# Performance work log

Hardware: AMD Instinct MI355X
Metric: run time of the kernel (lower is better)

## Reference

```python
import jax, jax.numpy as jnp
import numpy as np

N_NODES = 100000
N_EDGES = 1600000
D_IN = 128
D_HID = 128
D_OUT = 10
N_GRAPHS = 512


def _sage_conv(x, src, dst, W_l, b_l, W_r, num_nodes):
    # PyG SAGEConv (mean aggr): out = lin_l(mean_{j in N(i)} x_j) + lin_r(x_i)
    msg = x[src]                                            # [E, D] gather
    s = jax.ops.segment_sum(msg, dst, num_segments=num_nodes)
    cnt = jax.ops.segment_sum(jnp.ones((src.shape[0], 1), x.dtype), dst,
                              num_segments=num_nodes)
    mean = s / jnp.maximum(cnt, 1.0)                        # 0 where no neighbors
    return mean @ W_l.T + b_l + x @ W_r.T


def setup_inputs() -> dict:
    key = jax.random.key(0)
    ks = jax.random.split(key, 10)
    glorot = lambda k, o, i: jax.random.normal(k, (o, i), jnp.float32) * (1.0 / np.sqrt(i))
    return {
        "x": jax.random.normal(ks[0], (N_NODES, D_IN), jnp.float32),
        "edge_index": jax.random.randint(ks[1], (2, N_EDGES), 0, N_NODES, jnp.int64),
        "batch": jnp.sort(jax.random.randint(ks[2], (N_NODES,), 0, N_GRAPHS, jnp.int64)),
        "W1_l": glorot(ks[3], D_HID, D_IN),
        "b1": jnp.zeros((D_HID,), jnp.float32),
        "W1_r": glorot(ks[4], D_HID, D_IN),
        "W2_l": glorot(ks[5], D_HID, D_HID),
        "b2": jnp.zeros((D_HID,), jnp.float32),
        "W2_r": glorot(ks[6], D_HID, D_HID),
        "Wf": glorot(ks[7], D_OUT, D_HID),
        "bf": jnp.zeros((D_OUT,), jnp.float32),
    }


def reference(x, edge_index, batch, W1_l, b1, W1_r, W2_l, b2, W2_r, Wf, bf):
    src, dst = edge_index[0], edge_index[1]
    n = x.shape[0]
    h = jax.nn.relu(_sage_conv(x, src, dst, W1_l, b1, W1_r, n))
    h = jax.nn.relu(_sage_conv(h, src, dst, W2_l, b2, W2_r, n))
    # global_mean_pool over graph ids
    gsum = jax.ops.segment_sum(h, batch, num_segments=N_GRAPHS)
    gcnt = jax.ops.segment_sum(jnp.ones((n, 1), h.dtype), batch, num_segments=N_GRAPHS)
    g = gsum / jnp.maximum(gcnt, 1.0)
    logits = g @ Wf.T + bf
    return jax.nn.log_softmax(logits, axis=-1)
```

## Files before the change

### kernel.cpp

```cpp
#include <hip/hip_runtime.h>
#include <hip/hip_bf16.h>

#define N_NODES 100000
#define N_EDGES 1600000
#define N_GRAPHS 512
#define NB 256
#define NPB 391
#define CHUNK 6250
#define STAGE 7680

typedef __attribute__((ext_vector_type(8))) short short8;
typedef __attribute__((ext_vector_type(4))) float f32x4;
typedef __attribute__((ext_vector_type(2))) float f32x2;

__device__ __forceinline__ float b2f(ushort u) {
    union { unsigned int i; float f; } c; c.i = ((unsigned int)u) << 16; return c.f;
}
__device__ __forceinline__ float blo(unsigned int u) {
    union { unsigned int i; float f; } c; c.i = u << 16; return c.f;
}
__device__ __forceinline__ float bhi(unsigned int u) {
    union { unsigned int i; float f; } c; c.i = u & 0xffff0000u; return c.f;
}
__device__ __forceinline__ ushort f2b(float f) {
    union { float f; unsigned int i; } c; c.f = f;
    unsigned int r = (c.i + 0x7fffu + ((c.i >> 16) & 1u)) >> 16;
    return (ushort)r;
}
__device__ __forceinline__ int idx_at(const void* p, long i, int f) {
    return f ? (int)((const long long*)p)[i] : ((const int*)p)[i];
}
__device__ __forceinline__ short8 dec8(const uchar* p) {
    uint2 q = *(const uint2*)p;
    f32x2 d0 = __builtin_amdgcn_cvt_pk_f32_fp8((int)q.x, false);
    f32x2 d1 = __builtin_amdgcn_cvt_pk_f32_fp8((int)q.x, true);
    f32x2 d2 = __builtin_amdgcn_cvt_pk_f32_fp8((int)q.y, false);
    f32x2 d3 = __builtin_amdgcn_cvt_pk_f32_fp8((int)q.y, true);
    short8 s;
    s[0] = (short)f2b(d0.x); s[1] = (short)f2b(d0.y);
    s[2] = (short)f2b(d1.x); s[3] = (short)f2b(d1.y);
    s[4] = (short)f2b(d2.x); s[5] = (short)f2b(d2.y);
    s[6] = (short)f2b(d3.x); s[7] = (short)f2b(d3.y);
    return s;
}

__global__ __launch_bounds__(256) void k_detect(const unsigned int* __restrict__ xw,
                                                const unsigned int* __restrict__ ew,
                                                const int* __restrict__ bw,
                                                int* __restrict__ flags) {
    __shared__ int cf, ce, cb;
    int t = threadIdx.x;
    if (t == 0) { cf = 0; ce = 0; cb = 0; }
    __syncthreads();
    unsigned int w = xw[t];
    unsigned int e = (w >> 7) & 0xffu;
    if (e >= 110u && e <= 130u) atomicAdd(&cf, 1);
    if (t < 128) {
        if (ew[2 * t + 1] != 0u) atomicAdd(&ce, 1);
        if (bw[99001 + 2 * t] != 0) atomicAdd(&cb, 1);
    }
    __syncthreads();
    if (t == 0) {
        flags[0] = (cf >= 128) ? 1 : 0;
        flags[1] = (ce == 0) ? 1 : 0;
        flags[2] = (cb == 0) ? 1 : 0;
    }
}

__global__ __launch_bounds__(256) void k_prep(const void* __restrict__ ei,
                                              const void* __restrict__ x,
                                              ushort* __restrict__ xbf,
                                              unsigned int* __restrict__ xf8,
                                              const void* W1l, const void* W1r,
                                              const void* W2l, const void* W2r,
                                              const void* b1,  const void* b2,
                                              ushort* __restrict__ wbf,
                                              int* __restrict__ blkcnt,
                                              const int* __restrict__ flags) {
    int b = blockIdx.x, t = threadIdx.x;
    if (b < NB) {
        __shared__ int h[NB];
        int f = flags[1];
        for (int j = t; j < NB; j += 256) h[j] = 0;
        __syncthreads();
        int lo = b * CHUNK, hi = lo + CHUNK;
        for (int e = lo + t; e < hi; e += 256) {
            int d = idx_at(ei, (long)N_EDGES + e, f);
            atomicAdd(&h[d / NPB], 1);
        }
        __syncthreads();
        if (t < NB) blkcnt[b * NB + t] = h[t];
    } else if (b < NB + 2048) {
        bool f32src = (flags[0] == 0);
        int vb = b - NB;
        const long nG = (long)N_NODES * 128 / 4;
        for (long g = (long)vb * 256 + t; g < nG; g += 2048L * 256) {
            float v0, v1, v2, v3;
            if (f32src) {
                float4 vv = ((const float4*)x)[g];
                v0 = vv.x; v1 = vv.y; v2 = vv.z; v3 = vv.w;
                unsigned int lo = (unsigned int)f2b(v0) | ((unsigned int)f2b(v1) << 16);
                unsigned int hi = (unsigned int)f2b(v2) | ((unsigned int)f2b(v3) << 16);
                ((uint2*)xbf)[g] = make_uint2(lo, hi);
            } else {
                uint2 q = ((const uint2*)x)[g];
                v0 = blo(q.x); v1 = bhi(q.x); v2 = blo(q.y); v3 = bhi(q.y);
            }
            int r = __builtin_amdgcn_cvt_pk_fp8_f32(v0, v1, 0, false);
            r = __builtin_amdgcn_cvt_pk_fp8_f32(v2, v3, r, true);
            xf8[g] = (unsigned int)r;
        }
    } else {
        int idx = (b - NB - 2048) * 256 + t;
        if (idx >= 65792) return;
        const void* src; int off;
        if      (idx < 16384) { src = W1l; off = idx; }
        else if (idx < 32768) { src = W1r; off = idx - 16384; }
        else if (idx < 49152) { src = W2l; off = idx - 32768; }
        else if (idx < 65536) { src = W2r; off = idx - 49152; }
        else if (idx < 65664) { src = b1;  off = idx - 65536; }
        else                  { src = b2;  off = idx - 65664; }
        wbf[idx] = (flags[0] != 0) ? ((const ushort*)src)[off]
                                   : f2b(((const float*)src)[off]);
    }
}

__global__ __launch_bounds__(NB) void k_bscan(const int* __restrict__ blkcnt,
                                              int* __restrict__ bucketBase,
                                              int* __restrict__ blkbase) {
    __shared__ int s[NB];
    int t = threadIdx.x;
    int tot = 0;
    for (int blk = 0; blk < NB; ++blk) tot += blkcnt[blk * NB + t];
    s[t] = tot; __syncthreads();
    for (int off = 1; off < NB; off <<= 1) {
        int a = (t >= off) ? s[t - off] : 0;
        __syncthreads();
        s[t] += a;
        __syncthreads();
    }
    int excl = s[t] - tot;
    bucketBase[t] = excl;
    if (t == NB - 1) bucketBase[NB] = s[NB - 1];
    int run = excl;
    for (int blk = 0; blk < NB; ++blk) {
        blkbase[blk * NB + t] = run;
        run += blkcnt[blk * NB + t];
    }
}

__global__ __launch_bounds__(256) void k_bin(const void* __restrict__ ei,
                                             const int* __restrict__ blkbase,
                                             int* __restrict__ binned,
                                             const int* __restrict__ flags) {
    __shared__ int bb[NB];
    __shared__ int rank[NB];
    int t = threadIdx.x, blk = blockIdx.x;
    int f = flags[1];
    for (int j = t; j < NB; j += 256) { bb[j] = blkbase[blk * NB + j]; rank[j] = 0; }
    __syncthreads();
    int lo = blk * CHUNK, hi = lo + CHUNK;
    for (int e = lo + t; e < hi; e += 256) {
        int s = idx_at(ei, e, f);
        int d = idx_at(ei, (long)N_EDGES + e, f);
        int b = d / NPB;
        int loc = d - b * NPB;
        int r = atomicAdd(&rank[b], 1);
        binned[bb[b] + r] = s | (loc << 20);
    }
}

__global__ __launch_bounds__(256) void k_csr(const int* __restrict__ binned,
                                             const int* __restrict__ bucketBase,
                                             int* __restrict__ rowptr,
                                             int* __restrict__ csr) {
    __shared__ int cnt[400];
    __shared__ int sc[400];
    __shared__ int sh[256];
    __shared__ int stage[STAGE];
    int t = threadIdx.x, b = blockIdx.x;
    int nodeLo = b * NPB;
    int nC = N_NODES - nodeLo; if (nC > NPB) nC = NPB;
    int eBase = bucketBase[b], eEnd = bucketBase[b + 1];

    for (int j = t; j < 400; j += 256) cnt[j] = 0;
    __syncthreads();
    for (int i = eBase + t; i < eEnd; i += 256)
        atomicAdd(&cnt[binned[i] >> 20], 1);
    __syncthreads();
    int base = t * 2;
    int v0 = (base < 400) ? cnt[base] : 0;
    int v1 = (base + 1 < 400) ? cnt[base + 1] : 0;
    int ssum = v0 + v1;
    sh[t] = ssum; __syncthreads();
    for (int off = 1; off < 256; off <<= 1) {
        int a = (t >= off) ? sh[t - off] : 0;
        __syncthreads();
        sh[t] += a;
        __syncthreads();
    }
    int pre = sh[t] - ssum;
    if (base < 400) sc[base] = pre;
    if (base + 1 < 400) sc[base + 1] = pre + v0;
    __syncthreads();
    for (int j = t; j < nC; j += 256) rowptr[nodeLo + j] = eBase + sc[j];
    if (b == NB - 1) {
        if (t == 0) rowptr[N_NODES] = eEnd;
        if (t < 64) csr[N_EDGES + t] = 0;
    }
    for (int j = t; j < 400; j += 256) cnt[j] = 0;
    __syncthreads();
    for (int i = eBase + t; i < eEnd; i += 256) {
        int p = binned[i];
        int loc = p >> 20;
        int pos = sc[loc] + atomicAdd(&cnt[loc], 1);
        int srcn = p & 0xFFFFF;
        if (pos < STAGE) stage[pos] = srcn;
        else csr[eBase + pos] = srcn;
    }
    __syncthreads();
    int eCnt = eEnd - eBase; if (eCnt > STAGE) eCnt = STAGE;
    for (int j = t; j < eCnt; j += 256) csr[eBase + j] = stage[j];
}

__global__ __launch_bounds__(256) void k_agg(const uint2* __restrict__ x16,
                                             const int* __restrict__ rowptr,
                                             const int* __restrict__ csr,
                                             uint2* __restrict__ mout) {
    int wv = blockIdx.x * 4 + (threadIdx.x >> 6);
    int lane = threadIdx.x & 63;
    int li = lane & 15;
    int node = wv * 4 + (lane >> 4);
    int beg = rowptr[node];
    int end = rowptr[node + 1];
    int deg = end - beg;
    int m = deg;
    m = max(m, __shfl_xor(m, 16));
    m = max(m, __shfl_xor(m, 32));
    int degmax = __builtin_amdgcn_readfirstlane(m);
    float a0 = 0.f, a1 = 0.f, a2 = 0.f, a3 = 0.f;
    float a4 = 0.f, a5 = 0.f, a6 = 0.f, a7 = 0.f;
    for (int j = 0; j < degmax; j += 16) {
        int pos = beg + j + li;
        if (pos > end - 1) pos = (deg > 0) ? end - 1 : 0;
        int vidx = csr[pos];
#pragma unroll
        for (int c = 0; c < 16; c += 8) {
            if (j + c >= degmax) break;
            uint2 p[8];
#pragma unroll
            for (int i = 0; i < 8; ++i) {
                int idx = __shfl(vidx, (c + i) | (lane & 48));
                p[i] = x16[(long)idx * 16 + li];
            }
#pragma unroll
            for (int i = 0; i < 8; ++i) {
                bool ok = (j + c + i < deg);
                unsigned int qx = ok ? p[i].x : 0u;
                unsigned int qy = ok ? p[i].y : 0u;
                f32x2 d0 = __builtin_amdgcn_cvt_pk_f32_fp8((int)qx, false);
                f32x2 d1 = __builtin_amdgcn_cvt_pk_f32_fp8((int)qx, true);
                f32x2 d2 = __builtin_amdgcn_cvt_pk_f32_fp8((int)qy, false);
                f32x2 d3 = __builtin_amdgcn_cvt_pk_f32_fp8((int)qy, true);
                a0 += d0.x; a1 += d0.y; a2 += d1.x; a3 += d1.y;
                a4 += d2.x; a5 += d2.y; a6 += d3.x; a7 += d3.y;
            }
        }
    }
    float s = (deg > 0) ? 1.f / (float)deg : 0.f;
    int r0 = __builtin_amdgcn_cvt_pk_fp8_f32(a0 * s, a1 * s, 0, false);
    r0 = __builtin_amdgcn_cvt_pk_fp8_f32(a2 * s, a3 * s, r0, true);
    int r1 = __builtin_amdgcn_cvt_pk_fp8_f32(a4 * s, a5 * s, 0, false);
    r1 = __builtin_amdgcn_cvt_pk_fp8_f32(a6 * s, a7 * s, r1, true);
    mout[(long)node * 16 + li] = make_uint2((unsigned int)r0, (unsigned int)r1);
}

__global__ __launch_bounds__(256) void k_gemm(const uchar* __restrict__ A0f8,
                                              const ushort* __restrict__ A1a,
                                              const ushort* __restrict__ A1b,
                                              const uchar* __restrict__ A1f8,
                                              const ushort* __restrict__ Wl,
                                              const ushort* __restrict__ Wr,
                                              const ushort* __restrict__ bias,
                                              ushort* __restrict__ outb,
                                              uchar* __restrict__ out8,
                                              const int* __restrict__ flags,
                                              int layer1) {
    __shared__ short Ws[4096 * 8];
    int t = threadIdx.x;
    const ushort* A1 = flags[0] ? A1a : A1b;
#pragma unroll
    for (int i = 0; i < 16; ++i) {
        int f = i * 256 + t;
        int lane = f & 63, kk = (f >> 6) & 7, tile = f >> 9;
        int o = tile * 16 + (lane & 15);
        int k0 = kk * 32 + ((lane >> 4) * 8);
        const ushort* wsrc = (k0 < 128) ? (Wl + o * 128 + k0)
                                        : (Wr + o * 128 + (k0 - 128));
        *(short8*)&Ws[f * 8] = *(const short8*)wsrc;
    }
    __syncthreads();

    int wid = t >> 6, lane = t & 63;
    long nbase = (long)blockIdx.x * 64 + (long)wid * 16;
    int arow = (int)nbase + (lane & 15);
    if (arow >= N_NODES) arow = N_NODES - 1;
    int kq = (lane >> 4) * 8;

    short8 afrag[8];
#pragma unroll
    for (int kk = 0; kk < 8; ++kk) {
        int k0 = kk * 32 + kq;
        if (k0 < 128) {
            afrag[kk] = dec8(A0f8 + (long)arow * 128 + k0);
        } else if (layer1) {
            afrag[kk] = *(const short8*)(A1 + (long)arow * 128 + (k0 - 128));
        } else {
            afrag[kk] = dec8(A1f8 + (long)arow * 128 + (k0 - 128));
        }
    }

#pragma unroll
    for (int tile = 0; tile < 8; ++tile) {
        f32x4 acc = {0.f, 0.f, 0.f, 0.f};
#pragma unroll
        for (int kk = 0; kk < 8; ++kk) {
            short8 bfrag = *(short8*)&Ws[((tile * 8 + kk) * 64 + lane) * 8];
            acc = __builtin_amdgcn_mfma_f32_16x16x32_bf16(afrag[kk], bfrag, acc, 0, 0, 0);
        }
        int o = tile * 16 + (lane & 15);
        float bo = b2f(bias[o]);
#pragma unroll
        for (int r = 0; r < 4; ++r) {
            long node = nbase + (lane >> 4) * 4 + r;
            if (node < N_NODES) {
                float v = acc[r] + bo;
                v = v > 0.f ? v : 0.f;
                if (layer1) {
                    int pp = __builtin_amdgcn_cvt_pk_fp8_f32(v, v, 0, false);
                    out8[node * 128 + o] = (uchar)pp;
                } else {
                    outb[node * 128 + o] = f2b(v);
                }
            }
        }
    }
}

__global__ __launch_bounds__(256) void k_pool_cls(const ushort* __restrict__ h2,
                                                  const void* __restrict__ batch,
                                                  const void* __restrict__ Wf,
                                                  const void* __restrict__ bfv,
                                                  void* __restrict__ outp,
                                                  const int* __restrict__ flags) {
    int g = blockIdx.x, t = threadIdx.x;
    int wid = t >> 6, lane = t & 63;
    bool f32 = (flags[0] == 0);
    int b64 = flags[2];
    __shared__ int rng[2];
    __shared__ float redA[4][64];
    __shared__ float redB[4][64];
    __shared__ float gv[128];
    __shared__ float lg[10];
    if (t < 2) {
        int v = g + t, lo = 0, hi = N_NODES;
        while (lo < hi) {
            int mid = (lo + hi) >> 1;
            if (idx_at(batch, mid, b64) < v) lo = mid + 1; else hi = mid;
        }
        rng[t] = lo;
    }
    __syncthreads();
    int lo = rng[0], hi = rng[1];
    const unsigned int* xr = (const unsigned int*)h2;
    float a0 = 0.f, a1 = 0.f;
    int n = lo + wid;
    for (; n + 28 < hi; n += 32) {
        unsigned int p[8];
#pragma unroll
        for (int i = 0; i < 8; ++i) p[i] = xr[(long)(n + i * 4) * 64 + lane];
#pragma unroll
        for (int i = 0; i < 8; ++i) { a0 += blo(p[i]); a1 += bhi(p[i]); }
    }
    for (; n < hi; n += 4) {
        unsigned int q = xr[(long)n * 64 + lane];
        a0 += blo(q); a1 += bhi(q);
    }
    redA[wid][lane] = a0;
    redB[wid][lane] = a1;
    __syncthreads();
    if (wid == 0) {
        float s0 = redA[0][lane] + redA[1][lane] + redA[2][lane] + redA[3][lane];
        float s1 = redB[0][lane] + redB[1][lane] + redB[2][lane] + redB[3][lane];
        float c = (hi > lo) ? (float)(hi - lo) : 1.f;
        gv[lane * 2]     = s0 / c;
        gv[lane * 2 + 1] = s1 / c;
    }
    __syncthreads();
    if (t < 10) {
        float s = f32 ? ((const float*)bfv)[t] : b2f(((const ushort*)bfv)[t]);
        for (int k = 0; k < 128; ++k) {
            float wv = f32 ? ((const float*)Wf)[t * 128 + k] : b2f(((const ushort*)Wf)[t * 128 + k]);
            s += gv[k] * wv;
        }
        lg[t] = s;
    }
    __syncthreads();
    if (t == 0) {
        float mx = lg[0];
        for (int i = 1; i < 10; ++i) mx = fmaxf(mx, lg[i]);
        float se = 0.f;
        for (int i = 0; i < 10; ++i) se += expf(lg[i] - mx);
        float lse = mx + logf(se);
        for (int i = 0; i < 10; ++i) {
            float v = lg[i] - lse;
            if (f32) ((float*)outp)[g * 10 + i] = v;
            else     ((ushort*)outp)[g * 10 + i] = f2b(v);
        }
    }
}

extern "C" void kernel_launch(void* const* d_in, const int* in_sizes, int n_in,
                              void* d_out, int out_size, void* d_ws, size_t ws_size,
                              hipStream_t stream) {
    const void* x     = d_in[0];
    const void* ei    = d_in[1];
    const void* batch = d_in[2];
    const void* W1l = d_in[3];
    const void* b1  = d_in[4];
    const void* W1r = d_in[5];
    const void* W2l = d_in[6];
    const void* b2  = d_in[7];
    const void* W2r = d_in[8];
    const void* Wf  = d_in[9];
    const void* bf_ = d_in[10];

    char* w = (char*)d_ws;
    int* flags      = (int*)(w + 0);
    int* rowptr     = (int*)(w + 640);
    ushort* wbf     = (ushort*)(w + 400768);
    int* csr        = (int*)(w + 532480);
    ushort* xbf     = (ushort*)(w + 6933248);
    ushort* h2      = (ushort*)(w + 6933248);
    uchar* mbuf     = (uchar*)(w + 32533248);
    int* bucketBase = (int*)(w + 32533248);
    int* blkcnt     = (int*)(w + 32534528);
    int* blkbase    = (int*)(w + 32796672);
    uchar* h1f8     = (uchar*)(w + 58133248);
    int* binned     = (int*)(w + 58133248);
    unsigned int* xf8 = (unsigned int*)(w + 70933248);

    dim3 blk256(256), blkNB(NB);

    k_detect<<<1, blk256, 0, stream>>>((const unsigned int*)x, (const unsigned int*)ei,
                                       (const int*)batch, flags);
    k_prep<<<NB + 2048 + 257, blk256, 0, stream>>>(ei, x, xbf, xf8,
                                                   W1l, W1r, W2l, W2r, b1, b2,
                                                   wbf, blkcnt, flags);
    k_bscan<<<1, blkNB, 0, stream>>>(blkcnt, bucketBase, blkbase);
    k_bin<<<NB, blk256, 0, stream>>>(ei, blkbase, binned, flags);
    k_csr<<<NB, blk256, 0, stream>>>(binned, bucketBase, rowptr, csr);

    int agrid = N_NODES / 4 / 4;
    int ggrid = (N_NODES + 63) / 64;

    k_agg<<<agrid, blk256, 0, stream>>>((const uint2*)xf8, rowptr, csr, (uint2*)mbuf);
    k_gemm<<<ggrid, blk256, 0, stream>>>(mbuf, (const ushort*)x, xbf, (const uchar*)nullptr,
                                         wbf + 0, wbf + 16384, wbf + 65536,
                                         (ushort*)nullptr, h1f8, flags, 1);
    k_agg<<<agrid, blk256, 0, stream>>>((const uint2*)h1f8, rowptr, csr, (uint2*)mbuf);
    k_gemm<<<ggrid, blk256, 0, stream>>>(mbuf, (const ushort*)x, xbf, h1f8,
                                         wbf + 32768, wbf + 49152, wbf + 65664,
                                         h2, (uchar*)nullptr, flags, 0);
    k_pool_cls<<<N_GRAPHS, blk256, 0, stream>>>(h2, batch, Wf, bf_, d_out, flags);
}
```

Baseline: 319.4 us.

## Fuse mean pooling into layer-2 GEMM epilogue and widen aggregation loads

The second GEMM now accumulates ReLU outputs directly into per-graph sums. It uses LDS atomics when a 64-node block spans few graphs and global atomics otherwise, which removes the bf16 h2 write and the pooling kernel's reread of it. The classifier kernel now only normalizes the sums and applies the final linear and log-softmax. Separately, the aggregation kernel assigns 8 lanes per node with 16-byte fp8 loads instead of 16 lanes with 8-byte loads. The tradeoffs are float atomics with nondeterministic summation order, an extra memset, and more accumulator registers in aggregation.

```diff
diff --git a/kernel.cpp b/kernel.cpp
--- a/kernel.cpp
+++ b/kernel.cpp
@@ -223,56 +223,65 @@
     for (int j = t; j < eCnt; j += 256) csr[eBase + j] = stage[j];
 }
 
-__global__ __launch_bounds__(256) void k_agg(const uint2* __restrict__ x16,
+__global__ __launch_bounds__(256) void k_agg(const uint4* __restrict__ x8,
                                              const int* __restrict__ rowptr,
                                              const int* __restrict__ csr,
-                                             uint2* __restrict__ mout) {
+                                             uint4* __restrict__ mout) {
     int wv = blockIdx.x * 4 + (threadIdx.x >> 6);
     int lane = threadIdx.x & 63;
-    int li = lane & 15;
-    int node = wv * 4 + (lane >> 4);
+    int li = lane & 7;
+    int node = wv * 8 + (lane >> 3);
     int beg = rowptr[node];
     int end = rowptr[node + 1];
     int deg = end - beg;
     int m = deg;
+    m = max(m, __shfl_xor(m, 8));
     m = max(m, __shfl_xor(m, 16));
     m = max(m, __shfl_xor(m, 32));
     int degmax = __builtin_amdgcn_readfirstlane(m);
-    float a0 = 0.f, a1 = 0.f, a2 = 0.f, a3 = 0.f;
-    float a4 = 0.f, a5 = 0.f, a6 = 0.f, a7 = 0.f;
-    for (int j = 0; j < degmax; j += 16) {
+    float a[16];
+#pragma unroll
+    for (int i = 0; i < 16; ++i) a[i] = 0.f;
+    for (int j = 0; j < degmax; j += 8) {
         int pos = beg + j + li;
         if (pos > end - 1) pos = (deg > 0) ? end - 1 : 0;
         int vidx = csr[pos];
-#pragma unroll
-        for (int c = 0; c < 16; c += 8) {
-            if (j + c >= degmax) break;
-            uint2 p[8];
-#pragma unroll
-            for (int i = 0; i < 8; ++i) {
-                int idx = __shfl(vidx, (c + i) | (lane & 48));
-                p[i] = x16[(long)idx * 16 + li];
-            }
-#pragma unroll
-            for (int i = 0; i < 8; ++i) {
-                bool ok = (j + c + i < deg);
-                unsigned int qx = ok ? p[i].x : 0u;
-                unsigned int qy = ok ? p[i].y : 0u;
-                f32x2 d0 = __builtin_amdgcn_cvt_pk_f32_fp8((int)qx, false);
-                f32x2 d1 = __builtin_amdgcn_cvt_pk_f32_fp8((int)qx, true);
-                f32x2 d2 = __builtin_amdgcn_cvt_pk_f32_fp8((int)qy, false);
-                f32x2 d3 = __builtin_amdgcn_cvt_pk_f32_fp8((int)qy, true);
-                a0 += d0.x; a1 += d0.y; a2 += d1.x; a3 += d1.y;
-                a4 += d2.x; a5 += d2.y; a6 += d3.x; a7 += d3.y;
-            }
+        uint4 p[8];
+#pragma unroll
+        for (int i = 0; i < 8; ++i) {
+            int idx = __shfl(vidx, i | (lane & 56));
+            p[i] = x8[(long)idx * 8 + li];
+        }
+#pragma unroll
+        for (int i = 0; i < 8; ++i) {
+            bool ok = (j + i < deg);
+            unsigned int q0 = ok ? p[i].x : 0u;
+            unsigned int q1 = ok ? p[i].y : 0u;
+            unsigned int q2 = ok ? p[i].z : 0u;
+            unsigned int q3 = ok ? p[i].w : 0u;
+            f32x2 d;
+            d = __builtin_amdgcn_cvt_pk_f32_fp8((int)q0, false); a[0] += d.x;  a[1] += d.y;
+            d = __builtin_amdgcn_cvt_pk_f32_fp8((int)q0, true);  a[2] += d.x;  a[3] += d.y;
+            d = __builtin_amdgcn_cvt_pk_f32_fp8((int)q1, false); a[4] += d.x;  a[5] += d.y;
+            d = __builtin_amdgcn_cvt_pk_f32_fp8((int)q1, true);  a[6] += d.x;  a[7] += d.y;
+            d = __builtin_amdgcn_cvt_pk_f32_fp8((int)q2, false); a[8] += d.x;  a[9] += d.y;
+            d = __builtin_amdgcn_cvt_pk_f32_fp8((int)q2, true);  a[10] += d.x; a[11] += d.y;
+            d = __builtin_amdgcn_cvt_pk_f32_fp8((int)q3, false); a[12] += d.x; a[13] += d.y;
+            d = __builtin_amdgcn_cvt_pk_f32_fp8((int)q3, true);  a[14] += d.x; a[15] += d.y;
         }
     }
     float s = (deg > 0) ? 1.f / (float)deg : 0.f;
-    int r0 = __builtin_amdgcn_cvt_pk_fp8_f32(a0 * s, a1 * s, 0, false);
-    r0 = __builtin_amdgcn_cvt_pk_fp8_f32(a2 * s, a3 * s, r0, true);
-    int r1 = __builtin_amdgcn_cvt_pk_fp8_f32(a4 * s, a5 * s, 0, false);
-    r1 = __builtin_amdgcn_cvt_pk_fp8_f32(a6 * s, a7 * s, r1, true);
-    mout[(long)node * 16 + li] = make_uint2((unsigned int)r0, (unsigned int)r1);
+    uint4 o;
+    int r;
+    r = __builtin_amdgcn_cvt_pk_fp8_f32(a[0] * s, a[1] * s, 0, false);
+    r = __builtin_amdgcn_cvt_pk_fp8_f32(a[2] * s, a[3] * s, r, true);  o.x = (unsigned int)r;
+    r = __builtin_amdgcn_cvt_pk_fp8_f32(a[4] * s, a[5] * s, 0, false);
+    r = __builtin_amdgcn_cvt_pk_fp8_f32(a[6] * s, a[7] * s, r, true);  o.y = (unsigned int)r;
+    r = __builtin_amdgcn_cvt_pk_fp8_f32(a[8] * s, a[9] * s, 0, false);
+    r = __builtin_amdgcn_cvt_pk_fp8_f32(a[10] * s, a[11] * s, r, true); o.z = (unsigned int)r;
+    r = __builtin_amdgcn_cvt_pk_fp8_f32(a[12] * s, a[13] * s, 0, false);
+    r = __builtin_amdgcn_cvt_pk_fp8_f32(a[14] * s, a[15] * s, r, true); o.w = (unsigned int)r;
+    mout[(long)node * 8 + li] = o;
 }
 
 __global__ __launch_bounds__(256) void k_gemm(const uchar* __restrict__ A0f8,
@@ -282,13 +291,18 @@
                                               const ushort* __restrict__ Wl,
                                               const ushort* __restrict__ Wr,
                                               const ushort* __restrict__ bias,
-                                              ushort* __restrict__ outb,
                                               uchar* __restrict__ out8,
+                                              float* __restrict__ gsum,
+                                              const void* __restrict__ batch,
                                               const int* __restrict__ flags,
                                               int layer1) {
     __shared__ short Ws[4096 * 8];
+    __shared__ float gacc[8 * 128];
     int t = threadIdx.x;
     const ushort* A1 = flags[0] ? A1a : A1b;
+    if (!layer1) {
+        for (int j = t; j < 1024; j += 256) gacc[j] = 0.f;
+    }
 #pragma unroll
     for (int i = 0; i < 16; ++i) {
         int f = i * 256 + t;
@@ -320,6 +334,23 @@
         }
     }
 
+    int b64 = flags[2];
+    int gmin = 0, gspan = 0;
+    bool useLDS = true;
+    int gr[4];
+    if (!layer1) {
+        int first = blockIdx.x * 64;
+        int last = first + 63; if (last > N_NODES - 1) last = N_NODES - 1;
+        gmin = idx_at(batch, first, b64);
+        gspan = idx_at(batch, last, b64) - gmin;
+        useLDS = (gspan < 8);
+#pragma unroll
+        for (int r = 0; r < 4; ++r) {
+            long node = nbase + (lane >> 4) * 4 + r;
+            gr[r] = (node < N_NODES) ? idx_at(batch, node, b64) : 0;
+        }
+    }
+
 #pragma unroll
     for (int tile = 0; tile < 8; ++tile) {
         f32x4 acc = {0.f, 0.f, 0.f, 0.f};
@@ -339,27 +370,35 @@
                 if (layer1) {
                     int pp = __builtin_amdgcn_cvt_pk_fp8_f32(v, v, 0, false);
                     out8[node * 128 + o] = (uchar)pp;
+                } else if (useLDS) {
+                    atomicAdd(&gacc[(gr[r] - gmin) * 128 + o], v);
                 } else {
-                    outb[node * 128 + o] = f2b(v);
+                    atomicAdd(&gsum[gr[r] * 128 + o], v);
                 }
             }
         }
     }
-}
-
-__global__ __launch_bounds__(256) void k_pool_cls(const ushort* __restrict__ h2,
-                                                  const void* __restrict__ batch,
-                                                  const void* __restrict__ Wf,
-                                                  const void* __restrict__ bfv,
-                                                  void* __restrict__ outp,
-                                                  const int* __restrict__ flags) {
+
+    if (!layer1 && useLDS) {
+        __syncthreads();
+        int tot = (gspan + 1) * 128;
+        for (int j = t; j < tot; j += 256) {
+            float v = gacc[j];
+            if (v != 0.f) atomicAdd(&gsum[(gmin + (j >> 7)) * 128 + (j & 127)], v);
+        }
+    }
+}
+
+__global__ __launch_bounds__(128) void k_cls(const float* __restrict__ gsum,
+                                             const void* __restrict__ batch,
+                                             const void* __restrict__ Wf,
+                                             const void* __restrict__ bfv,
+                                             void* __restrict__ outp,
+                                             const int* __restrict__ flags) {
     int g = blockIdx.x, t = threadIdx.x;
-    int wid = t >> 6, lane = t & 63;
     bool f32 = (flags[0] == 0);
     int b64 = flags[2];
     __shared__ int rng[2];
-    __shared__ float redA[4][64];
-    __shared__ float redB[4][64];
     __shared__ float gv[128];
     __shared__ float lg[10];
     if (t < 2) {
@@ -371,31 +410,9 @@
         rng[t] = lo;
     }
     __syncthreads();
-    int lo = rng[0], hi = rng[1];
-    const unsigned int* xr = (const unsigned int*)h2;
-    float a0 = 0.f, a1 = 0.f;
-    int n = lo + wid;
-    for (; n + 28 < hi; n += 32) {
-        unsigned int p[8];
-#pragma unroll
-        for (int i = 0; i < 8; ++i) p[i] = xr[(long)(n + i * 4) * 64 + lane];
-#pragma unroll
-        for (int i = 0; i < 8; ++i) { a0 += blo(p[i]); a1 += bhi(p[i]); }
-    }
-    for (; n < hi; n += 4) {
-        unsigned int q = xr[(long)n * 64 + lane];
-        a0 += blo(q); a1 += bhi(q);
-    }
-    redA[wid][lane] = a0;
-    redB[wid][lane] = a1;
-    __syncthreads();
-    if (wid == 0) {
-        float s0 = redA[0][lane] + redA[1][lane] + redA[2][lane] + redA[3][lane];
-        float s1 = redB[0][lane] + redB[1][lane] + redB[2][lane] + redB[3][lane];
-        float c = (hi > lo) ? (float)(hi - lo) : 1.f;
-        gv[lane * 2]     = s0 / c;
-        gv[lane * 2 + 1] = s1 / c;
-    }
+    int cnt = rng[1] - rng[0];
+    float c = (cnt > 0) ? (float)cnt : 1.f;
+    gv[t] = gsum[g * 128 + t] / c;
     __syncthreads();
     if (t < 10) {
         float s = f32 ? ((const float*)bfv)[t] : b2f(((const ushort*)bfv)[t]);
@@ -441,7 +458,6 @@
     ushort* wbf     = (ushort*)(w + 400768);
     int* csr        = (int*)(w + 532480);
     ushort* xbf     = (ushort*)(w + 6933248);
-    ushort* h2      = (ushort*)(w + 6933248);
     uchar* mbuf     = (uchar*)(w + 32533248);
     int* bucketBase = (int*)(w + 32533248);
     int* blkcnt     = (int*)(w + 32534528);
@@ -449,8 +465,11 @@
     uchar* h1f8     = (uchar*)(w + 58133248);
     int* binned     = (int*)(w + 58133248);
     unsigned int* xf8 = (unsigned int*)(w + 70933248);
-
-    dim3 blk256(256), blkNB(NB);
+    float* gsum     = (float*)(w + 83733248);
+
+    dim3 blk256(256), blkNB(NB), blk128(128);
+
+    hipMemsetAsync(gsum, 0, N_GRAPHS * 128 * sizeof(float), stream);
 
     k_detect<<<1, blk256, 0, stream>>>((const unsigned int*)x, (const unsigned int*)ei,
                                        (const int*)batch, flags);
@@ -461,16 +480,16 @@
     k_bin<<<NB, blk256, 0, stream>>>(ei, blkbase, binned, flags);
     k_csr<<<NB, blk256, 0, stream>>>(binned, bucketBase, rowptr, csr);
 
-    int agrid = N_NODES / 4 / 4;
+    int agrid = N_NODES / 8 / 4;
     int ggrid = (N_NODES + 63) / 64;
 
-    k_agg<<<agrid, blk256, 0, stream>>>((const uint2*)xf8, rowptr, csr, (uint2*)mbuf);
+    k_agg<<<agrid, blk256, 0, stream>>>((const uint4*)xf8, rowptr, csr, (uint4*)mbuf);
     k_gemm<<<ggrid, blk256, 0, stream>>>(mbuf, (const ushort*)x, xbf, (const uchar*)nullptr,
                                          wbf + 0, wbf + 16384, wbf + 65536,
-                                         (ushort*)nullptr, h1f8, flags, 1);
-    k_agg<<<agrid, blk256, 0, stream>>>((const uint2*)h1f8, rowptr, csr, (uint2*)mbuf);
+                                         h1f8, (float*)nullptr, batch, flags, 1);
+    k_agg<<<agrid, blk256, 0, stream>>>((const uint4*)h1f8, rowptr, csr, (uint4*)mbuf);
     k_gemm<<<ggrid, blk256, 0, stream>>>(mbuf, (const ushort*)x, xbf, h1f8,
                                          wbf + 32768, wbf + 49152, wbf + 65664,
-                                         h2, (uchar*)nullptr, flags, 0);
-    k_pool_cls<<<N_GRAPHS, blk256, 0, stream>>>(h2, batch, Wf, bf_, d_out, flags);
-}
+                                         (uchar*)nullptr, gsum, batch, flags, 0);
+    k_cls<<<N_GRAPHS, blk128, 0, stream>>>(gsum, batch, Wf, bf_, d_out, flags);
+}
```

Result: slower. 388.6 us (+21.7%).
